# Optimization experiments

Measured on AMD Instinct MI355X. Metric: run time of the kernel, lower is better.

## Reference

```python
import jax, jax.numpy as jnp
import numpy as np

N_NODES = 50000
N_EDGES = 800000
IN_DIM = 128
OUT_DIM = 128
NUM_RELS = 100
NUM_BASES = 4


def setup_inputs() -> dict:
    key = jax.random.key(0)
    ks = jax.random.split(key, 8)
    h = jax.random.normal(ks[0], (N_NODES, IN_DIM), dtype=jnp.float32)
    norm = jax.random.uniform(ks[1], (N_NODES, 1), dtype=jnp.float32)
    src = jax.random.randint(ks[2], (N_EDGES,), 0, N_NODES, dtype=jnp.int32)
    dst = jax.random.randint(ks[3], (N_EDGES,), 0, N_NODES, dtype=jnp.int32)
    rel_type = jax.random.randint(ks[4], (N_EDGES,), 0, NUM_RELS, dtype=jnp.int32)
    basis_weights = jax.random.normal(ks[5], (NUM_BASES, IN_DIM, OUT_DIM), dtype=jnp.float32) * (2.0 / np.sqrt(IN_DIM + OUT_DIM))
    coefficients = jax.random.normal(ks[6], (NUM_RELS, NUM_BASES), dtype=jnp.float32) * (1.0 / np.sqrt(NUM_RELS + NUM_BASES))
    loop_weight = jax.random.normal(ks[7], (IN_DIM, OUT_DIM), dtype=jnp.float32) * (2.0 / np.sqrt(IN_DIM + OUT_DIM))
    return {
        'h': h, 'norm': norm, 'src': src, 'dst': dst, 'rel_type': rel_type,
        'basis_weights': basis_weights, 'coefficients': coefficients,
        'loop_weight': loop_weight,
    }


def reference(h, norm, src, dst, rel_type, basis_weights, coefficients, loop_weight):
    # h: (N, in), norm: (N, 1), src/dst/rel_type: (E,)
    # basis_weights: (B, in, out), coefficients: (R, B), loop_weight: (in, out)
    n_nodes = h.shape[0]
    num_bases = basis_weights.shape[0]

    # self-loop message (dropout=0 -> identity)
    loop_message = h @ loop_weight  # (N, out)

    # W[r] = sum_b coeff[r, b] * basis[b]; per-edge msg_e = h[src_e] @ W[rel_e].
    # Reassociated: project nodes by each basis once, then mix per edge by
    # the relation coefficients -- identical math, avoids the (E, in, out)
    # gathered weight tensor of the original per-edge bmm.
    hb = jnp.einsum('ni,bio->bno', h, basis_weights)  # (B, N, out)
    c_e = coefficients[rel_type]  # (E, B)
    msg = c_e[:, 0, None] * hb[0][src]
    for b in range(1, num_bases):  # small fixed basis count
        msg = msg + c_e[:, b, None] * hb[b][src]  # (E, out)

    # scatter-sum aggregation to destination nodes, then norm scaling
    agg = jax.ops.segment_sum(msg, dst, num_segments=n_nodes)  # (N, out)
    node_repr = agg * norm  # _apply_func
    node_repr = node_repr + loop_message  # self-loop (bias=None)
    return jax.nn.relu(node_repr)  # activation
```

## Files before the change

### kernel.cpp

```cpp
#include <hip/hip_runtime.h>

typedef short bf16x8 __attribute__((ext_vector_type(8)));
typedef float floatx4 __attribute__((ext_vector_type(4)));
typedef float floatx2 __attribute__((ext_vector_type(2)));

typedef const __attribute__((address_space(1))) void* gas_ptr;
typedef __attribute__((address_space(3))) void* las_ptr;

#define EPB  4096
#define MAXB 6144

__device__ __forceinline__ unsigned short f2bf(float f) {
    unsigned int u = __float_as_uint(f);
    unsigned int r = u + 0x7fffu + ((u >> 16) & 1u);
    return (unsigned short)(r >> 16);
}

__device__ __forceinline__ void stage16(const void* g, void* lbase, int lane) {
#if __has_builtin(__builtin_amdgcn_global_load_lds)
    __builtin_amdgcn_global_load_lds((gas_ptr)g, (las_ptr)lbase, 16, 0, 0);
#else
    *(float4*)((char*)lbase + lane * 16) = *(const float4*)g;
#endif
}

__global__ __launch_bounds__(1024) void prep_all(
    const float* __restrict__ h, unsigned short* __restrict__ hbf, int nconv8,
    const int* __restrict__ dst, const int* __restrict__ src,
    const int* __restrict__ rel, int* __restrict__ bcnt,
    unsigned int* __restrict__ tmp, int E, int nB, int nblkH,
    const float* __restrict__ basis, const float* __restrict__ loopw,
    unsigned short* __restrict__ WT2, int nb_conv)
{
    __shared__ int lh[256], cur[256];
    const int b = blockIdx.x;
    const int t = threadIdx.x;
    if (b < nb_conv) {
        int idx = b * 1024 + t;
        if (idx < nconv8) {
            const float4 v0 = *(const float4*)(h + (size_t)idx * 8);
            const float4 v1 = *(const float4*)(h + (size_t)idx * 8 + 4);
            uint4 p;
            p.x = (unsigned int)f2bf(v0.x) | ((unsigned int)f2bf(v0.y) << 16);
            p.y = (unsigned int)f2bf(v0.z) | ((unsigned int)f2bf(v0.w) << 16);
            p.z = (unsigned int)f2bf(v1.x) | ((unsigned int)f2bf(v1.y) << 16);
            p.w = (unsigned int)f2bf(v1.z) | ((unsigned int)f2bf(v1.w) << 16);
            *(uint4*)(hbf + (size_t)idx * 8) = p;
        }
    } else if (b < nb_conv + nblkH) {
        const int blk = b - nb_conv;
        if (t < 256) lh[t] = 0;
        __syncthreads();
        const int cbase = blk * EPB;
        int dd[EPB / 1024];
#pragma unroll
        for (int j = 0; j < EPB / 1024; ++j) {
            int e = cbase + j * 1024 + t;
            dd[j] = (e < E) ? dst[e] : -1;
            if (dd[j] >= 0) atomicAdd(&lh[dd[j] >> 8], 1);
        }
        __syncthreads();
        if (t < 256) {
            int c = lh[t];
            int base = c ? atomicAdd(&bcnt[t * 16], c) : 0;
            cur[t] = t * MAXB + base;
        }
        __syncthreads();
#pragma unroll
        for (int j = 0; j < EPB / 1024; ++j) {
            int e = cbase + j * 1024 + t;
            int d = dd[j];
            if (d >= 0) {
                int bin = d >> 8;
                int slot = atomicAdd(&cur[bin], 1);
                if (slot < (bin + 1) * MAXB)
                    tmp[slot] = (unsigned int)src[e]
                              | ((unsigned int)rel[e] << 16)
                              | ((unsigned int)(d & 255) << 23);
            }
        }
    } else {
        int c = b - nb_conv - nblkH;
        if (t < 640) {
            float v;
            if (t < 512) v = basis[(size_t)t * 128 + c];
            else         v = loopw[(size_t)(t - 512) * 128 + c];
            WT2[(size_t)c * 640 + t] = f2bf(v);
        }
    }
}

__global__ __launch_bounds__(1024) void bucket_sort(
    const unsigned int* __restrict__ tmp, const int* __restrict__ bcnt,
    unsigned int* __restrict__ sedge, int* __restrict__ rowptr,
    int E, int N, int nB)
{
    __shared__ unsigned int eb[MAXB];
    __shared__ int hh[256], ss[256], cur[256];
    __shared__ int sbrow, scnt;
    const int b = blockIdx.x;
    const int t = threadIdx.x;

    int c = 0;
    if (t < 256) {
        c = (t < nB) ? bcnt[t * 16] : 0;
        if (c > MAXB) c = MAXB;
        ss[t] = c;
    }
    __syncthreads();
    for (int o = 1; o < 256; o <<= 1) {
        int x = 0;
        if (t < 256 && t >= o) x = ss[t - o];
        __syncthreads();
        if (t < 256) ss[t] += x;
        __syncthreads();
    }
    if (t == b) { sbrow = ss[t] - c; scnt = c; }
    __syncthreads();
    const int brow = sbrow;
    const int n    = scnt;

    if (t < 256) hh[t] = 0;
    __syncthreads();
    const unsigned int* tb = tmp + (size_t)b * MAXB;
    for (int i = t; i < n; i += 1024) {
        unsigned int v = tb[i];
        eb[i] = v;
        atomicAdd(&hh[(v >> 23) & 255], 1);
    }
    __syncthreads();
    int v = 0;
    if (t < 256) { v = hh[t]; ss[t] = v; }
    __syncthreads();
    for (int o = 1; o < 256; o <<= 1) {
        int x = 0;
        if (t < 256 && t >= o) x = ss[t - o];
        __syncthreads();
        if (t < 256) ss[t] += x;
        __syncthreads();
    }
    if (t < 256) {
        const int excl = ss[t] - v;
        const int idx = b * 256 + t;
        if (idx <= N) rowptr[idx] = brow + excl;
        cur[t] = excl;
    }
    __syncthreads();
    for (int i = t; i < n; i += 1024) {
        unsigned int e = eb[i];
        int slot = atomicAdd(&cur[(e >> 23) & 255], 1);
        sedge[brow + slot] = ((e & 0xFFFFu) << 8) | (((e >> 16) & 0x7Fu) << 25);
    }
}

__global__ __launch_bounds__(256, 8) void aggregate_pre(
    const unsigned short* __restrict__ hbf,
    const int* __restrict__ rowptr,
    const unsigned int* __restrict__ sedge,
    const float* __restrict__ coeff,
    const float* __restrict__ norm,
    unsigned short* __restrict__ A2, int N, int R)
{
    __shared__ float scoef[512];
    for (int i = threadIdx.x; i < R * 4; i += 256) scoef[i] = coeff[i];
    __syncthreads();

    const int wave = threadIdx.x >> 6;
    const int lane = threadIdx.x & 63;
    const int d = blockIdx.x * 4 + wave;
    if (d >= N) return;
    int i = rowptr[d];
    const int end = rowptr[d + 1];

    const char* hbase = (const char*)hbf + lane * 4;

    floatx2 a0 = {0.f, 0.f}, a1 = {0.f, 0.f}, a2 = {0.f, 0.f}, a3 = {0.f, 0.f};

#define EDGE_LOAD(v, u) \
    unsigned int u = *(const unsigned int*)(hbase + ((v) & 0x00FFFF00u));
#define EDGE_MATH(v, u) { \
    const float4 c = *(const float4*)((const char*)scoef + (((v) >> 25) << 4)); \
    floatx2 hp; \
    hp[0] = __uint_as_float((u) << 16); \
    hp[1] = __uint_as_float((u) & 0xFFFF0000u); \
    a0 = __builtin_elementwise_fma((floatx2){c.x, c.x}, hp, a0); \
    a1 = __builtin_elementwise_fma((floatx2){c.y, c.y}, hp, a1); \
    a2 = __builtin_elementwise_fma((floatx2){c.z, c.z}, hp, a2); \
    a3 = __builtin_elementwise_fma((floatx2){c.w, c.w}, hp, a3); }

    while (i < end && (i & 3)) {
        unsigned int v = sedge[i];
        EDGE_LOAD(v, u)
        EDGE_MATH(v, u)
        ++i;
    }
    for (; i + 16 <= end; i += 16) {
        uint4 e0 = *(const uint4*)(sedge + i);
        uint4 e1 = *(const uint4*)(sedge + i + 4);
        uint4 e2 = *(const uint4*)(sedge + i + 8);
        uint4 e3 = *(const uint4*)(sedge + i + 12);
        EDGE_LOAD(e0.x, u0)  EDGE_LOAD(e0.y, u1)  EDGE_LOAD(e0.z, u2)  EDGE_LOAD(e0.w, u3)
        EDGE_LOAD(e1.x, u4)  EDGE_LOAD(e1.y, u5)  EDGE_LOAD(e1.z, u6)  EDGE_LOAD(e1.w, u7)
        EDGE_LOAD(e2.x, u8)  EDGE_LOAD(e2.y, u9)  EDGE_LOAD(e2.z, u10) EDGE_LOAD(e2.w, u11)
        EDGE_LOAD(e3.x, u12) EDGE_LOAD(e3.y, u13) EDGE_LOAD(e3.z, u14) EDGE_LOAD(e3.w, u15)
        EDGE_MATH(e0.x, u0)  EDGE_MATH(e0.y, u1)  EDGE_MATH(e0.z, u2)  EDGE_MATH(e0.w, u3)
        EDGE_MATH(e1.x, u4)  EDGE_MATH(e1.y, u5)  EDGE_MATH(e1.z, u6)  EDGE_MATH(e1.w, u7)
        EDGE_MATH(e2.x, u8)  EDGE_MATH(e2.y, u9)  EDGE_MATH(e2.z, u10) EDGE_MATH(e2.w, u11)
        EDGE_MATH(e3.x, u12) EDGE_MATH(e3.y, u13) EDGE_MATH(e3.z, u14) EDGE_MATH(e3.w, u15)
    }
    for (; i + 8 <= end; i += 8) {
        uint4 e0 = *(const uint4*)(sedge + i);
        uint4 e1 = *(const uint4*)(sedge + i + 4);
        EDGE_LOAD(e0.x, u0) EDGE_LOAD(e0.y, u1) EDGE_LOAD(e0.z, u2) EDGE_LOAD(e0.w, u3)
        EDGE_LOAD(e1.x, u4) EDGE_LOAD(e1.y, u5) EDGE_LOAD(e1.z, u6) EDGE_LOAD(e1.w, u7)
        EDGE_MATH(e0.x, u0) EDGE_MATH(e0.y, u1) EDGE_MATH(e0.z, u2) EDGE_MATH(e0.w, u3)
        EDGE_MATH(e1.x, u4) EDGE_MATH(e1.y, u5) EDGE_MATH(e1.z, u6) EDGE_MATH(e1.w, u7)
    }
    for (; i + 4 <= end; i += 4) {
        uint4 e0 = *(const uint4*)(sedge + i);
        EDGE_LOAD(e0.x, u0) EDGE_LOAD(e0.y, u1) EDGE_LOAD(e0.z, u2) EDGE_LOAD(e0.w, u3)
        EDGE_MATH(e0.x, u0) EDGE_MATH(e0.y, u1) EDGE_MATH(e0.z, u2) EDGE_MATH(e0.w, u3)
    }
    for (; i < end; ++i) {
        unsigned int v = sedge[i];
        EDGE_LOAD(v, u)
        EDGE_MATH(v, u)
    }
#undef EDGE_LOAD
#undef EDGE_MATH

    const float nm = norm[d];
    unsigned short* row = A2 + (size_t)d * 512 + lane * 2;
    *(unsigned int*)(row)       = (unsigned int)f2bf(a0[0] * nm) | ((unsigned int)f2bf(a0[1] * nm) << 16);
    *(unsigned int*)(row + 128) = (unsigned int)f2bf(a1[0] * nm) | ((unsigned int)f2bf(a1[1] * nm) << 16);
    *(unsigned int*)(row + 256) = (unsigned int)f2bf(a2[0] * nm) | ((unsigned int)f2bf(a2[1] * nm) << 16);
    *(unsigned int*)(row + 384) = (unsigned int)f2bf(a3[0] * nm) | ((unsigned int)f2bf(a3[1] * nm) << 16);
}

__global__ __launch_bounds__(256) void final_gemm(
    const unsigned short* __restrict__ A2,
    const unsigned short* __restrict__ hbf,
    const unsigned short* __restrict__ WT2,
    float* __restrict__ out, int N)
{
    __shared__ char sA[16384];
    __shared__ char sB[16384];
    const int t = threadIdx.x;
    const int w = t >> 6;
    const int lane = t & 63;
    const int quad = lane >> 4;
    const int low  = lane & 15;
    const int wr = w >> 1, wc = w & 1;
    const int m0 = blockIdx.x * 128;

    floatx4 acc[4][4];
#pragma unroll
    for (int mt = 0; mt < 4; ++mt)
#pragma unroll
        for (int nt = 0; nt < 4; ++nt) acc[mt][nt] = (floatx4){0.f, 0.f, 0.f, 0.f};

    for (int it = 0; it < 10; ++it) {
        const int k0 = it * 64;
#pragma unroll
        for (int i = 0; i < 4; ++i) {
            const int slot = i * 256 + t;
            const int kc  = slot >> 7;
            const int idx = slot & 127;
            int grow = m0 + idx;
            if (grow >= N) grow = N - 1;
            const unsigned short* gA = (k0 < 512)
                ? A2  + (size_t)grow * 512 + k0 + kc * 8
                : hbf + (size_t)grow * 128 + (k0 - 512) + kc * 8;
            const unsigned short* gB = WT2 + (size_t)idx * 640 + k0 + kc * 8;
            stage16(gA, sA + (size_t)(i * 256 + w * 64) * 16, lane);
            stage16(gB, sB + (size_t)(i * 256 + w * 64) * 16, lane);
        }
        __syncthreads();

#pragma unroll
        for (int ks = 0; ks < 2; ++ks) {
            bf16x8 af[4], bfr[4];
#pragma unroll
            for (int mt = 0; mt < 4; ++mt)
                af[mt] = *(const bf16x8*)(sA + (size_t)(((ks * 4 + quad) << 7) + wr * 64 + mt * 16 + low) * 16);
#pragma unroll
            for (int nt = 0; nt < 4; ++nt)
                bfr[nt] = *(const bf16x8*)(sB + (size_t)(((ks * 4 + quad) << 7) + wc * 64 + nt * 16 + low) * 16);
#pragma unroll
            for (int mt = 0; mt < 4; ++mt)
#pragma unroll
                for (int nt = 0; nt < 4; ++nt)
                    acc[mt][nt] = __builtin_amdgcn_mfma_f32_16x16x32_bf16(af[mt], bfr[nt], acc[mt][nt], 0, 0, 0);
        }
        __syncthreads();
    }

#pragma unroll
    for (int mt = 0; mt < 4; ++mt) {
#pragma unroll
        for (int nt = 0; nt < 4; ++nt) {
            const int c = wc * 64 + nt * 16 + low;
#pragma unroll
            for (int r = 0; r < 4; ++r) {
                int rr = m0 + wr * 64 + mt * 16 + quad * 4 + r;
                if (rr < N) out[(size_t)rr * 128 + c] = fmaxf(acc[mt][nt][r], 0.f);
            }
        }
    }
}

extern "C" void kernel_launch(void* const* d_in, const int* in_sizes, int n_in,
                              void* d_out, int out_size, void* d_ws, size_t ws_size,
                              hipStream_t stream)
{
    const float* h     = (const float*)d_in[0];
    const float* norm  = (const float*)d_in[1];
    const int*   src   = (const int*)d_in[2];
    const int*   dst   = (const int*)d_in[3];
    const int*   rel   = (const int*)d_in[4];
    const float* basis = (const float*)d_in[5];
    const float* coeff = (const float*)d_in[6];
    const float* loopw = (const float*)d_in[7];
    float* out = (float*)d_out;

    const int N = in_sizes[1];
    const int E = in_sizes[2];
    const int R = in_sizes[6] / 4;

    const int nB    = (N + 255) >> 8;
    const int nblkH = (E + EPB - 1) / EPB;

    char* ws = (char*)d_ws;
    size_t off = 0;
    auto walloc = [&](size_t bytes) -> char* {
        char* p = ws + off;
        off = (off + bytes + 255) & ~(size_t)255;
        return p;
    };
    unsigned short* A2     = (unsigned short*)walloc((size_t)N * 512 * 2);
    unsigned short* hbf    = (unsigned short*)walloc((size_t)N * 128 * 2);
    unsigned short* WT2    = (unsigned short*)walloc(128 * 640 * 2);
    int*            rowptr = (int*)walloc((size_t)(N + 1) * 4);
    int*            bcnt   = (int*)walloc((size_t)nB * 16 * 4);
    unsigned int*   tmp    = (unsigned int*)walloc((size_t)nB * MAXB * 4);
    unsigned int*   sedge  = (unsigned int*)walloc((size_t)E * 4);

    const int nconv8  = N * 16;
    const int nb_conv = (nconv8 + 1023) / 1024;

    hipMemsetAsync(bcnt, 0, (size_t)nB * 16 * 4, stream);
    prep_all<<<nb_conv + nblkH + 128, 1024, 0, stream>>>(
        h, hbf, nconv8, dst, src, rel, bcnt, tmp, E, nB, nblkH,
        basis, loopw, WT2, nb_conv);
    bucket_sort<<<nB, 1024, 0, stream>>>(tmp, bcnt, sedge, rowptr, E, N, nB);
    aggregate_pre<<<(N + 3) / 4, 256, 0, stream>>>(hbf, rowptr, sedge, coeff, norm, A2, N, R);
    final_gemm<<<(N + 127) / 128, 256, 0, stream>>>(A2, hbf, WT2, out, N);
}
```

Measured before the change: 187.4 us.

## Split feature dim into 4 passes, process 4 edges per wave in parallel

```diff
diff --git a/kernel.cpp b/kernel.cpp
--- a/kernel.cpp
+++ b/kernel.cpp
@@ -167,14 +167,10 @@
 
     const int wave = threadIdx.x >> 6;
     const int lane = threadIdx.x & 63;
-    const int d = blockIdx.x * 4 + wave;
-    if (d >= N) return;
-    int i = rowptr[d];
-    const int end = rowptr[d + 1];
-
-    const char* hbase = (const char*)hbf + lane * 4;
-
-    floatx2 a0 = {0.f, 0.f}, a1 = {0.f, 0.f}, a2 = {0.f, 0.f}, a3 = {0.f, 0.f};
+    const int e4   = lane >> 4;
+    const int kd   = lane & 15;
+    const int gw = blockIdx.x * 4 + wave;
+    const int GW = gridDim.x * 4;
 
 #define EDGE_LOAD(v, u) \
     unsigned int u = *(const unsigned int*)(hbase + ((v) & 0x00FFFF00u));
@@ -188,53 +184,66 @@
     a2 = __builtin_elementwise_fma((floatx2){c.z, c.z}, hp, a2); \
     a3 = __builtin_elementwise_fma((floatx2){c.w, c.w}, hp, a3); }
 
-    while (i < end && (i & 3)) {
-        unsigned int v = sedge[i];
-        EDGE_LOAD(v, u)
-        EDGE_MATH(v, u)
-        ++i;
-    }
-    for (; i + 16 <= end; i += 16) {
-        uint4 e0 = *(const uint4*)(sedge + i);
-        uint4 e1 = *(const uint4*)(sedge + i + 4);
-        uint4 e2 = *(const uint4*)(sedge + i + 8);
-        uint4 e3 = *(const uint4*)(sedge + i + 12);
-        EDGE_LOAD(e0.x, u0)  EDGE_LOAD(e0.y, u1)  EDGE_LOAD(e0.z, u2)  EDGE_LOAD(e0.w, u3)
-        EDGE_LOAD(e1.x, u4)  EDGE_LOAD(e1.y, u5)  EDGE_LOAD(e1.z, u6)  EDGE_LOAD(e1.w, u7)
-        EDGE_LOAD(e2.x, u8)  EDGE_LOAD(e2.y, u9)  EDGE_LOAD(e2.z, u10) EDGE_LOAD(e2.w, u11)
-        EDGE_LOAD(e3.x, u12) EDGE_LOAD(e3.y, u13) EDGE_LOAD(e3.z, u14) EDGE_LOAD(e3.w, u15)
-        EDGE_MATH(e0.x, u0)  EDGE_MATH(e0.y, u1)  EDGE_MATH(e0.z, u2)  EDGE_MATH(e0.w, u3)
-        EDGE_MATH(e1.x, u4)  EDGE_MATH(e1.y, u5)  EDGE_MATH(e1.z, u6)  EDGE_MATH(e1.w, u7)
-        EDGE_MATH(e2.x, u8)  EDGE_MATH(e2.y, u9)  EDGE_MATH(e2.z, u10) EDGE_MATH(e2.w, u11)
-        EDGE_MATH(e3.x, u12) EDGE_MATH(e3.y, u13) EDGE_MATH(e3.z, u14) EDGE_MATH(e3.w, u15)
-    }
-    for (; i + 8 <= end; i += 8) {
-        uint4 e0 = *(const uint4*)(sedge + i);
-        uint4 e1 = *(const uint4*)(sedge + i + 4);
-        EDGE_LOAD(e0.x, u0) EDGE_LOAD(e0.y, u1) EDGE_LOAD(e0.z, u2) EDGE_LOAD(e0.w, u3)
-        EDGE_LOAD(e1.x, u4) EDGE_LOAD(e1.y, u5) EDGE_LOAD(e1.z, u6) EDGE_LOAD(e1.w, u7)
-        EDGE_MATH(e0.x, u0) EDGE_MATH(e0.y, u1) EDGE_MATH(e0.z, u2) EDGE_MATH(e0.w, u3)
-        EDGE_MATH(e1.x, u4) EDGE_MATH(e1.y, u5) EDGE_MATH(e1.z, u6) EDGE_MATH(e1.w, u7)
-    }
-    for (; i + 4 <= end; i += 4) {
-        uint4 e0 = *(const uint4*)(sedge + i);
-        EDGE_LOAD(e0.x, u0) EDGE_LOAD(e0.y, u1) EDGE_LOAD(e0.z, u2) EDGE_LOAD(e0.w, u3)
-        EDGE_MATH(e0.x, u0) EDGE_MATH(e0.y, u1) EDGE_MATH(e0.z, u2) EDGE_MATH(e0.w, u3)
-    }
-    for (; i < end; ++i) {
-        unsigned int v = sedge[i];
-        EDGE_LOAD(v, u)
-        EDGE_MATH(v, u)
+    for (int p = 0; p < 4; ++p) {
+        const char* hbase = (const char*)hbf + p * 64 + kd * 4;
+        for (int d = gw; d < N; d += GW) {
+            int i = rowptr[d];
+            const int end = rowptr[d + 1];
+
+            floatx2 a0 = {0.f, 0.f}, a1 = {0.f, 0.f}, a2 = {0.f, 0.f}, a3 = {0.f, 0.f};
+
+            for (; i + 16 <= end; i += 16) {
+                unsigned int v0 = sedge[i + e4];
+                unsigned int v1 = sedge[i + 4 + e4];
+                unsigned int v2 = sedge[i + 8 + e4];
+                unsigned int v3 = sedge[i + 12 + e4];
+                EDGE_LOAD(v0, u0) EDGE_LOAD(v1, u1) EDGE_LOAD(v2, u2) EDGE_LOAD(v3, u3)
+                EDGE_MATH(v0, u0) EDGE_MATH(v1, u1) EDGE_MATH(v2, u2) EDGE_MATH(v3, u3)
+            }
+            for (; i + 8 <= end; i += 8) {
+                unsigned int v0 = sedge[i + e4];
+                unsigned int v1 = sedge[i + 4 + e4];
+                EDGE_LOAD(v0, u0) EDGE_LOAD(v1, u1)
+                EDGE_MATH(v0, u0) EDGE_MATH(v1, u1)
+            }
+            for (; i + 4 <= end; i += 4) {
+                unsigned int v0 = sedge[i + e4];
+                EDGE_LOAD(v0, u0)
+                EDGE_MATH(v0, u0)
+            }
+            {
+                const int r = end - i;
+                if (e4 < r) {
+                    unsigned int v0 = sedge[i + e4];
+                    EDGE_LOAD(v0, u0)
+                    EDGE_MATH(v0, u0)
+                }
+            }
+
+#pragma unroll
+            for (int m = 16; m < 64; m <<= 1) {
+                a0[0] += __shfl_xor(a0[0], m); a0[1] += __shfl_xor(a0[1], m);
+                a1[0] += __shfl_xor(a1[0], m); a1[1] += __shfl_xor(a1[1], m);
+                a2[0] += __shfl_xor(a2[0], m); a2[1] += __shfl_xor(a2[1], m);
+                a3[0] += __shfl_xor(a3[0], m); a3[1] += __shfl_xor(a3[1], m);
+            }
+
+            if (lane < 16) {
+                const float nm = norm[d];
+                char* rowp = (char*)A2 + (size_t)d * 1024 + p * 64 + kd * 4;
+                unsigned int w0 = (unsigned int)f2bf(a0[0] * nm) | ((unsigned int)f2bf(a0[1] * nm) << 16);
+                unsigned int w1 = (unsigned int)f2bf(a1[0] * nm) | ((unsigned int)f2bf(a1[1] * nm) << 16);
+                unsigned int w2 = (unsigned int)f2bf(a2[0] * nm) | ((unsigned int)f2bf(a2[1] * nm) << 16);
+                unsigned int w3 = (unsigned int)f2bf(a3[0] * nm) | ((unsigned int)f2bf(a3[1] * nm) << 16);
+                __builtin_nontemporal_store(w0, (unsigned int*)(rowp));
+                __builtin_nontemporal_store(w1, (unsigned int*)(rowp + 256));
+                __builtin_nontemporal_store(w2, (unsigned int*)(rowp + 512));
+                __builtin_nontemporal_store(w3, (unsigned int*)(rowp + 768));
+            }
+        }
     }
 #undef EDGE_LOAD
 #undef EDGE_MATH
-
-    const float nm = norm[d];
-    unsigned short* row = A2 + (size_t)d * 512 + lane * 2;
-    *(unsigned int*)(row)       = (unsigned int)f2bf(a0[0] * nm) | ((unsigned int)f2bf(a0[1] * nm) << 16);
-    *(unsigned int*)(row + 128) = (unsigned int)f2bf(a1[0] * nm) | ((unsigned int)f2bf(a1[1] * nm) << 16);
-    *(unsigned int*)(row + 256) = (unsigned int)f2bf(a2[0] * nm) | ((unsigned int)f2bf(a2[1] * nm) << 16);
-    *(unsigned int*)(row + 384) = (unsigned int)f2bf(a3[0] * nm) | ((unsigned int)f2bf(a3[1] * nm) << 16);
 }
 
 __global__ __launch_bounds__(256) void final_gemm(
@@ -353,6 +362,6 @@
         h, hbf, nconv8, dst, src, rel, bcnt, tmp, E, nB, nblkH,
         basis, loopw, WT2, nb_conv);
     bucket_sort<<<nB, 1024, 0, stream>>>(tmp, bcnt, sedge, rowptr, E, N, nB);
-    aggregate_pre<<<(N + 3) / 4, 256, 0, stream>>>(hbf, rowptr, sedge, coeff, norm, A2, N, R);
+    aggregate_pre<<<2048, 256, 0, stream>>>(hbf, rowptr, sedge, coeff, norm, A2, N, R);
     final_gemm<<<(N + 127) / 128, 256, 0, stream>>>(A2, hbf, WT2, out, N);
 }
```

Measured after the change: 226.5 us. +20.9%, slower.
